# Optimization experiments

Measured on AMD Instinct MI355X. Metric: run time of the kernel, lower is better.

## Reference

```python
import jax, jax.numpy as jnp
import numpy as np

B = 64
E = 512          # latent_size / h_dim
H = 8            # num_heads
D = E // H       # head_dim
MAX_AGENTS = 254 # max(agents_per_sample) for the deterministic counts below
NEG = -1e9


def setup_inputs() -> dict:
    key = jax.random.key(0)
    k_x, k_wi, k_bi, k_wo, k_bo = jax.random.split(key, 5)
    # deterministic variable agent counts in [128, 254]; sum == 11531, max == 254
    agents = jnp.array([128 + (3 * i) % 129 for i in range(B)], dtype=jnp.int32)
    total = 11531
    att_in = jax.random.normal(k_x, (total, E), dtype=jnp.float32)
    # nn.MultiheadAttention params: packed in-proj [3E, E] + bias, out-proj [E, E] + bias
    w_in = jax.random.normal(k_wi, (3 * E, E), dtype=jnp.float32) * 0.02
    b_in = jax.random.normal(k_bi, (3 * E,), dtype=jnp.float32) * 0.02
    w_out = jax.random.normal(k_wo, (E, E), dtype=jnp.float32) * 0.02
    b_out = jax.random.normal(k_bo, (E,), dtype=jnp.float32) * 0.02
    return {"att_in": att_in, "w_in": w_in, "b_in": b_in,
            "w_out": w_out, "b_out": b_out, "agents_per_sample": agents}


def reference(att_in, w_in, b_in, w_out, b_out, agents_per_sample):
    S = MAX_AGENTS
    # scatter packed rows into padded [B, S, E] via a clipped gather (jit-safe)
    offsets = jnp.cumsum(agents_per_sample) - agents_per_sample      # [B]
    pos = jnp.arange(S, dtype=jnp.int32)
    mask = pos[None, :] < agents_per_sample[:, None]                 # [B, S] valid
    idx = jnp.clip(offsets[:, None] + pos[None, :], 0, att_in.shape[0] - 1)
    padded = jnp.where(mask[..., None], att_in[idx], 0.0)            # [B, S, E]

    # fused QKV projection (torch packed in_proj), dropout disabled (eval)
    qkv = padded @ w_in.T + b_in                                     # [B, S, 3E]
    q, k, v = jnp.split(qkv, 3, axis=-1)
    q = q.reshape(B, S, H, D)
    k = k.reshape(B, S, H, D)
    v = v.reshape(B, S, H, D)

    scores = jnp.einsum('bqhd,bkhd->bhqk', q, k) * (D ** -0.5)      # [B, H, S, S]
    scores = jnp.where(mask[:, None, None, :], scores, NEG)          # key_padding_mask
    attn = jax.nn.softmax(scores, axis=-1)
    ctx = jnp.einsum('bhqk,bkhd->bqhd', attn, v).reshape(B, S, E)
    out = ctx @ w_out.T + b_out                                      # [B, S, E]
    # torch returns only valid rows per sample; zero the padded rows instead
    return out * mask[..., None]
```

## Files before the change

### kernel.cpp

```cpp
#include <hip/hip_runtime.h>
#include <hip/hip_bf16.h>

typedef __attribute__((ext_vector_type(8))) short bf16x8;
typedef __attribute__((ext_vector_type(4))) float f32x4;
typedef __attribute__((ext_vector_type(4))) int i32x4;
typedef __attribute__((ext_vector_type(4))) unsigned short u16x4;
typedef __attribute__((ext_vector_type(4))) float fl4;

struct __attribute__((packed)) u16x4u { u16x4 v; };

__device__ __forceinline__ f32x4 mfma16(bf16x8 a, bf16x8 b, f32x4 c) {
    return __builtin_amdgcn_mfma_f32_16x16x32_bf16(a, b, c, 0, 0, 0);
}

__device__ __forceinline__ unsigned short f2b(float f) {
    unsigned u = __float_as_uint(f);
    unsigned r = (u + 0x7FFF + ((u >> 16) & 1)) >> 16;
    return (unsigned short)r;
}

__device__ __forceinline__ int bsearch_off(const int* s_off, int m) {
    int lo = 0, hi = 63;
    while (lo < hi) {
        int mid = (lo + hi + 1) >> 1;
        if (s_off[mid] <= m) lo = mid; else hi = mid - 1;
    }
    return lo;
}

__device__ __forceinline__ void gld_lds16(const __hip_bfloat16* g, __hip_bfloat16* l) {
    __builtin_amdgcn_global_load_lds(
        (const __attribute__((address_space(1))) void*)g,
        (__attribute__((address_space(3))) void*)l,
        16, 0, 0);
}

__global__ void k_prep(const unsigned short* __restrict__ src,
                       const void* __restrict__ b_in, const void* __restrict__ b_out,
                       const int* __restrict__ agents,
                       int* __restrict__ flag, int* __restrict__ offs,
                       float* __restrict__ bfi, float* __restrict__ bfo) {
    __shared__ int sh[256];
    __shared__ int sa[64];
    __shared__ int sflag;
    int tid = threadIdx.x;
    int h = 0;
    for (int i = tid; i < 16384; i += 256) {
        unsigned e = (src[i] >> 7) & 0xFF;
        if (e == 0xFF) h = 1;
    }
    sh[tid] = h;
    if (tid < 64) sa[tid] = agents[tid];
    __syncthreads();
    if (tid == 0) {
        int any = 0;
        for (int i = 0; i < 256; ++i) any |= sh[i];
        flag[0] = any;
        sflag = any;
    }
    if (tid < 64) {
        int ex = 0;
        for (int i = 0; i < 64; ++i) { int v = sa[i]; if (i < tid) ex += v; }
        offs[tid] = ex;
        if (tid == 63) offs[64] = ex + sa[63];
    }
    __syncthreads();
    int f = sflag;
    for (int i = tid; i < 1536; i += 256)
        bfi[i] = f ? ((const float*)b_in)[i]
                   : __bfloat162float(((const __hip_bfloat16*)b_in)[i]);
    for (int i = tid; i < 512; i += 256)
        bfo[i] = f ? ((const float*)b_out)[i]
                   : __bfloat162float(((const __hip_bfloat16*)b_out)[i]);
}

__global__ void k_zero(char* __restrict__ out, long long out_elems, const int* __restrict__ flag) {
    long long bytes = flag[0] ? out_elems * 4 : out_elems * 2;
    long long i = ((long long)blockIdx.x * 256 + threadIdx.x) * 16;
    if (i < bytes) *(i32x4*)(out + i) = (i32x4){0, 0, 0, 0};
}

__global__ void k_cast(const void* __restrict__ src, unsigned short* __restrict__ dst,
                       int n, const int* __restrict__ flag) {
    int i = (blockIdx.x * 256 + threadIdx.x) * 4;
    if (i >= n) return;
    u16x4 o;
    if (flag[0]) {
        fl4 v = *(const fl4*)((const float*)src + i);
        o[0] = f2b(v[0]); o[1] = f2b(v[1]); o[2] = f2b(v[2]); o[3] = f2b(v[3]);
    } else {
        o = *(const u16x4*)((const unsigned short*)src + i);
    }
    *(u16x4*)(dst + i) = o;
}

template<int LDA, bool MROWS>
__device__ __forceinline__ void gemm_core(
    const __hip_bfloat16* __restrict__ A,
    const __hip_bfloat16* __restrict__ W,
    int m0, int n0, int total,
    __hip_bfloat16* As, __hip_bfloat16* Ws,
    f32x4 acc[4][4], int tid)
{
    int lane = tid & 63, quad = lane >> 4, c = lane & 15;
    int wave = tid >> 6;
    int wr = wave >> 1, wc = wave & 1;

    int chunk0 = tid;
    int chunk1 = 256 + tid;
    int ar0 = m0 + (chunk0 >> 2); if (ar0 > total - 1) ar0 = total - 1;
    int ar1 = m0 + (chunk1 >> 2); if (ar1 > total - 1) ar1 = total - 1;
    const __hip_bfloat16* gA0 = A + (size_t)ar0 * LDA + (chunk0 & 3) * 8;
    const __hip_bfloat16* gA1 = A + (size_t)ar1 * LDA + (chunk1 & 3) * 8;
    const __hip_bfloat16* gW0 = W + (size_t)(n0 + (chunk0 >> 2)) * 512 + (chunk0 & 3) * 8;
    const __hip_bfloat16* gW1 = W + (size_t)(n0 + (chunk1 >> 2)) * 512 + (chunk1 & 3) * 8;
    __hip_bfloat16* lA0 = As + (size_t)(wave * 64) * 8;
    __hip_bfloat16* lA1 = As + (size_t)(256 + wave * 64) * 8;
    __hip_bfloat16* lW0 = Ws + (size_t)(wave * 64) * 8;
    __hip_bfloat16* lW1 = Ws + (size_t)(256 + wave * 64) * 8;

    for (int k0 = 0; k0 < 512; k0 += 32) {
        if (k0) __syncthreads();
        gld_lds16(gA0 + k0, lA0);
        gld_lds16(gA1 + k0, lA1);
        gld_lds16(gW0 + k0, lW0);
        gld_lds16(gW1 + k0, lW1);
        __syncthreads();
        bf16x8 af[4], wf[4];
#pragma unroll
        for (int t = 0; t < 4; ++t) {
            af[t] = *(const bf16x8*)(As + (size_t)(wr * 64 + t * 16 + c) * 32 + quad * 8);
            wf[t] = *(const bf16x8*)(Ws + (size_t)(wc * 64 + t * 16 + c) * 32 + quad * 8);
        }
#pragma unroll
        for (int i = 0; i < 4; ++i)
#pragma unroll
            for (int j = 0; j < 4; ++j)
                acc[i][j] = MROWS ? mfma16(af[i], wf[j], acc[i][j])
                                  : mfma16(wf[j], af[i], acc[i][j]);
    }
}

__global__ __launch_bounds__(256) void k_qkv(
    const __hip_bfloat16* __restrict__ A,
    const __hip_bfloat16* __restrict__ W,
    const float* __restrict__ bias,
    const int* __restrict__ offs,
    __hip_bfloat16* __restrict__ qk,
    __hip_bfloat16* __restrict__ vT,
    int total, int MT)
{
    __shared__ __hip_bfloat16 As[128 * 32];
    __shared__ __hip_bfloat16 Ws[128 * 32];
    __shared__ int s_off[65];
    int l = blockIdx.x;
    int inner = l >> 3;
    int cb = inner % 12;
    int rb = (l & 7) + 8 * (inner / 12);
    if (rb >= MT) return;
    int n0 = cb * 128;
    int m0 = rb * 128;
    int tid = threadIdx.x;
    if (tid < 65) s_off[tid] = offs[tid];
    int lane = tid & 63, quad = lane >> 4, c = lane & 15;
    int wave = tid >> 6, wr = wave >> 1, wc = wave & 1;
    f32x4 z = {0.f, 0.f, 0.f, 0.f};
    f32x4 acc[4][4] = {{z,z,z,z},{z,z,z,z},{z,z,z,z},{z,z,z,z}};

    if (n0 < 1024) {
        gemm_core<512, false>(A, W, m0, n0, total, As, Ws, acc, tid);
        fl4 bv4[4];
#pragma unroll
        for (int j = 0; j < 4; ++j)
            bv4[j] = *(const fl4*)&bias[n0 + wc * 64 + j * 16 + quad * 4];
#pragma unroll
        for (int i = 0; i < 4; ++i) {
            int m = m0 + wr * 64 + i * 16 + c;
            if (m >= total) continue;
            size_t row = (size_t)m * 1024;
#pragma unroll
            for (int j = 0; j < 4; ++j) {
                int col0 = n0 + wc * 64 + j * 16 + quad * 4;
                u16x4 o;
#pragma unroll
                for (int r = 0; r < 4; ++r) o[r] = f2b(acc[i][j][r] + bv4[j][r]);
                *(u16x4*)&qk[row + col0] = o;
            }
        }
    } else {
        gemm_core<512, true>(A, W, m0, n0, total, As, Ws, acc, tid);
        float bv[4];
#pragma unroll
        for (int j = 0; j < 4; ++j) bv[j] = bias[n0 + wc * 64 + j * 16 + c];
#pragma unroll
        for (int i = 0; i < 4; ++i) {
            int m_base = m0 + wr * 64 + i * 16 + quad * 4;
            if (m_base >= total) continue;
            int lo = bsearch_off(s_off, m_base);
            bool vec = (m_base + 3 < total) && (s_off[lo + 1] > m_base + 3);
            if (vec) {
                int vs = m_base - s_off[lo];
#pragma unroll
                for (int j = 0; j < 4; ++j) {
                    int vc = n0 - 1024 + wc * 64 + j * 16 + c;
                    size_t idx = ((size_t)(lo * 8 + (vc >> 6)) * 64 + (vc & 63)) * 256 + vs;
                    u16x4 o;
#pragma unroll
                    for (int r = 0; r < 4; ++r) o[r] = f2b(acc[i][j][r] + bv[j]);
                    ((u16x4u*)&vT[idx])->v = o;
                }
            } else {
#pragma unroll
                for (int r = 0; r < 4; ++r) {
                    int m = m_base + r;
                    if (m >= total) continue;
                    int lo2 = bsearch_off(s_off, m);
                    int vs2 = m - s_off[lo2];
#pragma unroll
                    for (int j = 0; j < 4; ++j) {
                        int vc = n0 - 1024 + wc * 64 + j * 16 + c;
                        vT[((size_t)(lo2 * 8 + (vc >> 6)) * 64 + (vc & 63)) * 256 + vs2] =
                            __float2bfloat16(acc[i][j][r] + bv[j]);
                    }
                }
            }
        }
    }
}

__global__ __launch_bounds__(64) void k_attn(
    __hip_bfloat16* __restrict__ qk,
    const __hip_bfloat16* __restrict__ vT,
    const int* __restrict__ agents,
    const int* __restrict__ offs)
{
    __shared__ __hip_bfloat16 P[16][264];
    int bh = blockIdx.x;
    int qt = blockIdx.y;
    int b = bh >> 3, h = bh & 7;
    int n = agents[b];
    int qtiles = (n + 15) >> 4;
    if (qt >= qtiles) return;
    int off = offs[b];
    int ktiles = qtiles;
    int kt_pad = (ktiles + 1) & ~1;
    int stmax = (ktiles + 1) >> 1;
    int lane = threadIdx.x;
    int quad = lane >> 4, c = lane & 15;
    const __hip_bfloat16* vbase = vT + (size_t)bh * 64 * 256;

    int q0 = qt * 16;
    int qr = q0 + c; if (qr > n - 1) qr = n - 1;
    const __hip_bfloat16* qp = qk + (size_t)(off + qr) * 1024 + h * 64 + quad * 8;
    bf16x8 aq0 = *(const bf16x8*)qp;
    bf16x8 aq1 = *(const bf16x8*)(qp + 32);

    const __hip_bfloat16* kg = qk + (size_t)off * 1024 + 512 + h * 64 + quad * 8;
    float sm[4] = {0.f, 0.f, 0.f, 0.f};
#pragma unroll
    for (int kt = 0; kt < 16; ++kt) {
        if (kt < ktiles) {
            int kr = kt * 16 + c;
            bool bad = kr >= n;
            if (kr > n - 1) kr = n - 1;
            const __hip_bfloat16* kp = kg + (size_t)kr * 1024;
            f32x4 zz = {0.f, 0.f, 0.f, 0.f};
            zz = mfma16(aq0, *(const bf16x8*)kp, zz);
            zz = mfma16(aq1, *(const bf16x8*)(kp + 32), zz);
#pragma unroll
            for (int r = 0; r < 4; ++r) {
                float p = bad ? 0.f : __expf(zz[r] * 0.125f);
                sm[r] += p;
                P[quad * 4 + r][kt * 16 + c] = __float2bfloat16(p);
            }
        } else if (kt < kt_pad) {
#pragma unroll
            for (int r = 0; r < 4; ++r)
                P[quad * 4 + r][kt * 16 + c] = __float2bfloat16(0.f);
        }
    }
#pragma unroll
    for (int r = 0; r < 4; ++r) {
        float v = sm[r];
        v += __shfl_xor(v, 1);
        v += __shfl_xor(v, 2);
        v += __shfl_xor(v, 4);
        v += __shfl_xor(v, 8);
        sm[r] = 1.0f / v;
    }
    f32x4 z = {0.f, 0.f, 0.f, 0.f};
    f32x4 O[4] = {z, z, z, z};
#pragma unroll
    for (int st = 0; st < 8; ++st) {
        if (st < stmax) {
            bf16x8 ap = *(const bf16x8*)&P[c][st * 32 + quad * 8];
#pragma unroll
            for (int dt = 0; dt < 4; ++dt) {
                const __hip_bfloat16* vp = vbase + (size_t)(c + 16 * dt) * 256 + st * 32 + quad * 8;
                O[dt] = mfma16(ap, *(const bf16x8*)vp, O[dt]);
            }
        }
    }
#pragma unroll
    for (int r = 0; r < 4; ++r) {
        int q = quad * 4 + r;
        if (q0 + q < n) {
            float iv = sm[r];
            size_t row = (size_t)(off + q0 + q) * 1024 + h * 64;
#pragma unroll
            for (int dt = 0; dt < 4; ++dt)
                qk[row + 16 * dt + c] = __float2bfloat16(O[dt][r] * iv);
        }
    }
}

__global__ __launch_bounds__(256) void k_out(
    const __hip_bfloat16* __restrict__ A,
    const __hip_bfloat16* __restrict__ W,
    const float* __restrict__ bias,
    const int* __restrict__ offs,
    void* __restrict__ out,
    const int* __restrict__ flag,
    int total, int MT)
{
    __shared__ __hip_bfloat16 As[128 * 32];
    __shared__ __hip_bfloat16 Ws[128 * 32];
    __shared__ int s_off[65];
    int l = blockIdx.x;
    int inner = l >> 3;
    int cb = inner & 3;
    int rb = (l & 7) + 8 * (inner >> 2);
    if (rb >= MT) return;
    int n0 = cb * 128;
    int m0 = rb * 128;
    int tid = threadIdx.x;
    if (tid < 65) s_off[tid] = offs[tid];
    f32x4 z = {0.f, 0.f, 0.f, 0.f};
    f32x4 acc[4][4] = {{z,z,z,z},{z,z,z,z},{z,z,z,z},{z,z,z,z}};
    gemm_core<1024, false>(A, W, m0, n0, total, As, Ws, acc, tid);

    int f32m = flag[0];
    int lane = tid & 63, quad = lane >> 4, c = lane & 15;
    int wave = tid >> 6, wr = wave >> 1, wc = wave & 1;
    fl4 bv4[4];
#pragma unroll
    for (int j = 0; j < 4; ++j)
        bv4[j] = *(const fl4*)&bias[n0 + wc * 64 + j * 16 + quad * 4];
#pragma unroll
    for (int i = 0; i < 4; ++i) {
        int m = m0 + wr * 64 + i * 16 + c;
        if (m >= total) continue;
        int lo = bsearch_off(s_off, m);
        int os_ = m - s_off[lo];
        size_t rowb = ((size_t)(lo * 254 + os_)) * 512;
#pragma unroll
        for (int j = 0; j < 4; ++j) {
            int col0 = n0 + wc * 64 + j * 16 + quad * 4;
            if (f32m) {
                fl4 o;
#pragma unroll
                for (int r = 0; r < 4; ++r) o[r] = acc[i][j][r] + bv4[j][r];
                *(fl4*)&((float*)out)[rowb + col0] = o;
            } else {
                u16x4 o;
#pragma unroll
                for (int r = 0; r < 4; ++r) o[r] = f2b(acc[i][j][r] + bv4[j][r]);
                *(u16x4*)&((__hip_bfloat16*)out)[rowb + col0] = o;
            }
        }
    }
}

extern "C" void kernel_launch(void* const* d_in, const int* in_sizes, int n_in,
                              void* d_out, int out_size, void* d_ws, size_t ws_size,
                              hipStream_t stream) {
    const void* att_in = d_in[0];
    const void* w_in   = d_in[1];
    const void* b_in   = d_in[2];
    const void* w_out  = d_in[3];
    const void* b_out  = d_in[4];
    const int* agents  = (const int*)d_in[5];
    int total = in_sizes[0] / 512;

    char* p = (char*)d_ws;
    int* flag  = (int*)p;                 p += 256;
    int* offs  = (int*)p;                 p += 512;
    float* bfi = (float*)p;               p += 1536 * 4;
    float* bfo = (float*)p;               p += 512 * 4;
    __hip_bfloat16* WinBf  = (__hip_bfloat16*)p;  p += (size_t)1536 * 512 * 2;
    __hip_bfloat16* WoutBf = (__hip_bfloat16*)p;  p += (size_t)512 * 512 * 2;
    __hip_bfloat16* Abf    = (__hip_bfloat16*)p;  p += (size_t)total * 512 * 2;
    __hip_bfloat16* qk     = (__hip_bfloat16*)p;  p += (size_t)total * 1024 * 2;
    __hip_bfloat16* vT     = (__hip_bfloat16*)p;  p += (size_t)64 * 8 * 64 * 256 * 2;

    int nA = total * 512, nWi = 1536 * 512, nWo = 512 * 512;

    k_prep<<<1, 256, 0, stream>>>((const unsigned short*)att_in, b_in, b_out,
                                  agents, flag, offs, bfi, bfo);
    long long zblocks = ((long long)out_size * 4 / 16 + 255) / 256;
    k_zero<<<(int)zblocks, 256, 0, stream>>>((char*)d_out, out_size, flag);
    k_cast<<<(nA / 4 + 255) / 256, 256, 0, stream>>>(att_in, (unsigned short*)Abf, nA, flag);
    k_cast<<<(nWi / 4 + 255) / 256, 256, 0, stream>>>(w_in, (unsigned short*)WinBf, nWi, flag);
    k_cast<<<(nWo / 4 + 255) / 256, 256, 0, stream>>>(w_out, (unsigned short*)WoutBf, nWo, flag);

    int MT = (total + 127) / 128;
    int MTpad = ((MT + 7) / 8) * 8;
    k_qkv<<<12 * MTpad, 256, 0, stream>>>(Abf, WinBf, bfi, offs, qk, vT, total, MT);
    k_attn<<<dim3(512, 16), 64, 0, stream>>>(qk, vT, agents, offs);
    k_out<<<4 * MTpad, 256, 0, stream>>>(qk, WoutBf, bfo, offs, d_out, flag, total, MT);
}
```

Before: 210.2 us.

## Restructure attention: one block per (batch,head), 4 waves reuse K/V across query tiles

Result: faster. 188.0 us (-10.6%).

```diff
diff --git a/kernel.cpp b/kernel.cpp
--- a/kernel.cpp
+++ b/kernel.cpp
@@ -5,6 +5,7 @@
 typedef __attribute__((ext_vector_type(4))) float f32x4;
 typedef __attribute__((ext_vector_type(4))) int i32x4;
 typedef __attribute__((ext_vector_type(4))) unsigned short u16x4;
+typedef __attribute__((ext_vector_type(2))) unsigned ui2;
 typedef __attribute__((ext_vector_type(4))) float fl4;
 
 struct __attribute__((packed)) u16x4u { u16x4 v; };
@@ -228,88 +229,102 @@
     }
 }
 
-__global__ __launch_bounds__(64) void k_attn(
+__global__ __launch_bounds__(256, 2) void k_attn(
     __hip_bfloat16* __restrict__ qk,
     const __hip_bfloat16* __restrict__ vT,
     const int* __restrict__ agents,
     const int* __restrict__ offs)
 {
-    __shared__ __hip_bfloat16 P[16][264];
+    __shared__ __attribute__((aligned(16))) char Pl[4][16 * 80];
     int bh = blockIdx.x;
-    int qt = blockIdx.y;
     int b = bh >> 3, h = bh & 7;
     int n = agents[b];
+    int off = offs[b];
     int qtiles = (n + 15) >> 4;
-    if (qt >= qtiles) return;
-    int off = offs[b];
-    int ktiles = qtiles;
-    int kt_pad = (ktiles + 1) & ~1;
-    int stmax = (ktiles + 1) >> 1;
-    int lane = threadIdx.x;
-    int quad = lane >> 4, c = lane & 15;
+    int stmax = (qtiles + 1) >> 1;
+    int tid = threadIdx.x;
+    int wave = tid >> 6, lane = tid & 63, quad = lane >> 4, c = lane & 15;
     const __hip_bfloat16* vbase = vT + (size_t)bh * 64 * 256;
-
-    int q0 = qt * 16;
-    int qr = q0 + c; if (qr > n - 1) qr = n - 1;
-    const __hip_bfloat16* qp = qk + (size_t)(off + qr) * 1024 + h * 64 + quad * 8;
-    bf16x8 aq0 = *(const bf16x8*)qp;
-    bf16x8 aq1 = *(const bf16x8*)(qp + 32);
-
+    char* Plw = &Pl[wave][0];
+
+    bf16x8 qB[4][2];
+    int nt = 0;
+#pragma unroll
+    for (int t = 0; t < 4; ++t) {
+        int qt = wave + 4 * t;
+        if (qt < qtiles) {
+            nt = t + 1;
+            int qr = qt * 16 + c; if (qr > n - 1) qr = n - 1;
+            const __hip_bfloat16* qp = qk + (size_t)(off + qr) * 1024 + h * 64 + quad * 8;
+            qB[t][0] = *(const bf16x8*)qp;
+            qB[t][1] = *(const bf16x8*)(qp + 32);
+        }
+    }
+
+    f32x4 z = {0.f, 0.f, 0.f, 0.f};
+    f32x4 O[4][4] = {{z,z,z,z},{z,z,z,z},{z,z,z,z},{z,z,z,z}};
+    float sm[4] = {0.f, 0.f, 0.f, 0.f};
     const __hip_bfloat16* kg = qk + (size_t)off * 1024 + 512 + h * 64 + quad * 8;
-    float sm[4] = {0.f, 0.f, 0.f, 0.f};
-#pragma unroll
-    for (int kt = 0; kt < 16; ++kt) {
-        if (kt < ktiles) {
-            int kr = kt * 16 + c;
-            bool bad = kr >= n;
-            if (kr > n - 1) kr = n - 1;
+
+    for (int st = 0; st < stmax; ++st) {
+        int k0 = st * 32;
+        bf16x8 kA[2][2];
+#pragma unroll
+        for (int ti = 0; ti < 2; ++ti) {
+            int kr = k0 + ti * 16 + c; if (kr > n - 1) kr = n - 1;
             const __hip_bfloat16* kp = kg + (size_t)kr * 1024;
-            f32x4 zz = {0.f, 0.f, 0.f, 0.f};
-            zz = mfma16(aq0, *(const bf16x8*)kp, zz);
-            zz = mfma16(aq1, *(const bf16x8*)(kp + 32), zz);
-#pragma unroll
-            for (int r = 0; r < 4; ++r) {
-                float p = bad ? 0.f : __expf(zz[r] * 0.125f);
-                sm[r] += p;
-                P[quad * 4 + r][kt * 16 + c] = __float2bfloat16(p);
+            kA[ti][0] = *(const bf16x8*)kp;
+            kA[ti][1] = *(const bf16x8*)(kp + 32);
+        }
+        bf16x8 vA[4];
+#pragma unroll
+        for (int dt = 0; dt < 4; ++dt)
+            vA[dt] = *(const bf16x8*)(vbase + (size_t)(dt * 16 + c) * 256 + k0 + quad * 8);
+
+#pragma unroll
+        for (int t = 0; t < 4; ++t) {
+            if (t < nt) {
+#pragma unroll
+                for (int ti = 0; ti < 2; ++ti) {
+                    f32x4 s = mfma16(kA[ti][0], qB[t][0], z);
+                    s = mfma16(kA[ti][1], qB[t][1], s);
+                    int kbase = k0 + ti * 16 + quad * 4;
+                    float p0 = (kbase + 0 < n) ? __expf(s[0] * 0.125f) : 0.f;
+                    float p1 = (kbase + 1 < n) ? __expf(s[1] * 0.125f) : 0.f;
+                    float p2 = (kbase + 2 < n) ? __expf(s[2] * 0.125f) : 0.f;
+                    float p3 = (kbase + 3 < n) ? __expf(s[3] * 0.125f) : 0.f;
+                    sm[t] += (p0 + p1) + (p2 + p3);
+                    ui2 dw;
+                    dw[0] = (unsigned)f2b(p0) | ((unsigned)f2b(p1) << 16);
+                    dw[1] = (unsigned)f2b(p2) | ((unsigned)f2b(p3) << 16);
+                    *(ui2*)(Plw + c * 80 + ti * 32 + quad * 8) = dw;
+                }
+                bf16x8 pB = *(const bf16x8*)(Plw + c * 80 + quad * 16);
+#pragma unroll
+                for (int dt = 0; dt < 4; ++dt)
+                    O[t][dt] = mfma16(vA[dt], pB, O[t][dt]);
             }
-        } else if (kt < kt_pad) {
-#pragma unroll
-            for (int r = 0; r < 4; ++r)
-                P[quad * 4 + r][kt * 16 + c] = __float2bfloat16(0.f);
-        }
-    }
-#pragma unroll
-    for (int r = 0; r < 4; ++r) {
-        float v = sm[r];
-        v += __shfl_xor(v, 1);
-        v += __shfl_xor(v, 2);
-        v += __shfl_xor(v, 4);
-        v += __shfl_xor(v, 8);
-        sm[r] = 1.0f / v;
-    }
-    f32x4 z = {0.f, 0.f, 0.f, 0.f};
-    f32x4 O[4] = {z, z, z, z};
-#pragma unroll
-    for (int st = 0; st < 8; ++st) {
-        if (st < stmax) {
-            bf16x8 ap = *(const bf16x8*)&P[c][st * 32 + quad * 8];
-#pragma unroll
-            for (int dt = 0; dt < 4; ++dt) {
-                const __hip_bfloat16* vp = vbase + (size_t)(c + 16 * dt) * 256 + st * 32 + quad * 8;
-                O[dt] = mfma16(ap, *(const bf16x8*)vp, O[dt]);
+        }
+    }
+
+#pragma unroll
+    for (int t = 0; t < 4; ++t) {
+        if (t < nt) {
+            float v = sm[t];
+            v += __shfl_xor(v, 16);
+            v += __shfl_xor(v, 32);
+            float iv = 1.0f / v;
+            int q = (wave + 4 * t) * 16 + c;
+            if (q < n) {
+                size_t row = (size_t)(off + q) * 1024 + h * 64;
+#pragma unroll
+                for (int dt = 0; dt < 4; ++dt) {
+                    u16x4 o;
+#pragma unroll
+                    for (int r = 0; r < 4; ++r) o[r] = f2b(O[t][dt][r] * iv);
+                    *(u16x4*)&qk[row + dt * 16 + quad * 4] = o;
+                }
             }
-        }
-    }
-#pragma unroll
-    for (int r = 0; r < 4; ++r) {
-        int q = quad * 4 + r;
-        if (q0 + q < n) {
-            float iv = sm[r];
-            size_t row = (size_t)(off + q0 + q) * 1024 + h * 64;
-#pragma unroll
-            for (int dt = 0; dt < 4; ++dt)
-                qk[row + 16 * dt + c] = __float2bfloat16(O[dt][r] * iv);
         }
     }
 }
@@ -406,6 +421,6 @@
     int MT = (total + 127) / 128;
     int MTpad = ((MT + 7) / 8) * 8;
     k_qkv<<<12 * MTpad, 256, 0, stream>>>(Abf, WinBf, bfi, offs, qk, vT, total, MT);
-    k_attn<<<dim3(512, 16), 64, 0, stream>>>(qk, vT, agents, offs);
+    k_attn<<<512, 256, 0, stream>>>(qk, vT, agents, offs);
     k_out<<<4 * MTpad, 256, 0, stream>>>(qk, WoutBf, bfo, offs, d_out, flag, total, MT);
 }
```
